# Kernel optimization log

Measured on AMD Instinct MI355X. Metric: run time of the kernel, lower is better.

## Reference

```python
import jax, jax.numpy as jnp
import numpy as np

V, H, T, B, S = 100000, 256, 11, 32, 512
START, STOP = 9, 10
NEG = -1000.0


def _lstm_dir(x, wih, whh, b, reverse):
    """One direction of one LSTM layer. x: [B,S,in] -> [B,S,H]. Gate order i,f,g,o (PyTorch)."""
    Bx = x.shape[0]
    Hh = whh.shape[1]
    xs = (jnp.einsum('bsi,gi->bsg', x, wih) + b).transpose(1, 0, 2)  # [S,B,4H]

    def step(carry, xt):
        h, c = carry
        g = xt + h @ whh.T
        i, f, gg, o = jnp.split(g, 4, axis=-1)
        c = jax.nn.sigmoid(f) * c + jax.nn.sigmoid(i) * jnp.tanh(gg)
        h = jax.nn.sigmoid(o) * jnp.tanh(c)
        return (h, c), h

    init = (jnp.zeros((Bx, Hh), x.dtype), jnp.zeros((Bx, Hh), x.dtype))
    _, hs = jax.lax.scan(step, init, xs, reverse=reverse)
    return hs.transpose(1, 0, 2)


def _viterbi(feats, trans):
    """Max-plus Viterbi decode. feats: [B,S,T]. trans[next,prev]."""
    Bx, Sx, Tx = feats.shape
    init = jnp.full((Bx, Tx), NEG, feats.dtype).at[:, START].set(0.0)

    def fwd_step(fv, feat_t):
        scores = fv[:, None, :] + trans[None, :, :]      # [B,next,prev]
        bp = jnp.argmax(scores, axis=2)                  # [B,T]
        fv = jnp.max(scores, axis=2) + feat_t
        return fv, bp

    fv, bptrs = jax.lax.scan(fwd_step, init, feats.transpose(1, 0, 2))  # bptrs [S,B,T]
    terminal = fv + trans[STOP][None, :]
    score = jnp.max(terminal, axis=1)
    last = jnp.argmax(terminal, axis=1)

    def back_step(tag, bp):
        prev = jnp.take_along_axis(bp, tag[:, None], axis=1)[:, 0]
        return prev, tag

    _, path = jax.lax.scan(back_step, last, bptrs, reverse=True)  # [S,B], path[t]=tag_t
    return score, path.T  # [B], [B,S]


def setup_inputs() -> dict:
    key = jax.random.key(0)
    ks = jax.random.split(key, 20)

    def n(k, shape, s=0.1):
        return jax.random.normal(k, shape, jnp.float32) * s

    inp = {}
    inp['x'] = jax.random.randint(ks[0], (B, S), 0, V, dtype=jnp.int32)
    inp['batch_seq_len'] = jnp.full((B,), S, jnp.int32)
    inp['emb'] = n(ks[1], (V, H), 1.0)
    # layer 0 (input H), layer 1 (input 2H); f/b directions; bias = b_ih + b_hh fused
    inp['wih0f'] = n(ks[2], (4 * H, H)); inp['whh0f'] = n(ks[3], (4 * H, H)); inp['b0f'] = n(ks[4], (4 * H,))
    inp['wih0b'] = n(ks[5], (4 * H, H)); inp['whh0b'] = n(ks[6], (4 * H, H)); inp['b0b'] = n(ks[7], (4 * H,))
    inp['wih1f'] = n(ks[8], (4 * H, 2 * H)); inp['whh1f'] = n(ks[9], (4 * H, H)); inp['b1f'] = n(ks[10], (4 * H,))
    inp['wih1b'] = n(ks[11], (4 * H, 2 * H)); inp['whh1b'] = n(ks[12], (4 * H, H)); inp['b1b'] = n(ks[13], (4 * H,))
    inp['w_out'] = n(ks[14], (T, 2 * H)); inp['b_out'] = n(ks[15], (T,))
    trans = jax.random.normal(ks[16], (T, T), jnp.float32)
    trans = trans.at[START, :].set(NEG).at[:, STOP].set(NEG)
    inp['trans'] = trans
    return inp


def reference(x, batch_seq_len, emb, wih0f, whh0f, b0f, wih0b, whh0b, b0b,
              wih1f, whh1f, b1f, wih1b, whh1b, b1b, w_out, b_out, trans):
    # batch_seq_len: all sequences full length -> pack/pad is a no-op
    xe = emb[x]                                            # [B,S,H]
    h = jnp.concatenate([_lstm_dir(xe, wih0f, whh0f, b0f, False),
                         _lstm_dir(xe, wih0b, whh0b, b0b, True)], axis=-1)
    h = jnp.concatenate([_lstm_dir(h, wih1f, whh1f, b1f, False),
                         _lstm_dir(h, wih1b, whh1b, b1b, True)], axis=-1)
    feats = jnp.einsum('bsh,th->bst', h, w_out) + b_out    # [B,S,T]
    score, tag_seq = _viterbi(feats, trans)
    return score, tag_seq
```

## Files before the change

### kernel.cpp

```cpp
#include <hip/hip_runtime.h>
#include <math.h>

#define SS 512
#define BB 32
#define HH 256
#define G4 1024
#define TT 11
#define NEGV (-1000.0f)

static const size_t OFF_XE    = 0;
static const size_t OFF_XS    = 16777216ull;
static const size_t OFF_H0    = OFF_XS + 134217728ull;
static const size_t OFF_H1    = OFF_H0 + 33554432ull;
static const size_t OFF_FEATS = OFF_H1 + 33554432ull;
static const size_t OFF_HGRP  = OFF_FEATS + 720896ull;

__device__ __forceinline__ float fsig(float x) {
  return __builtin_amdgcn_rcpf(1.f + __expf(-x));
}
__device__ __forceinline__ float ftanh(float x) {
  return 1.f - 2.f * __builtin_amdgcn_rcpf(__expf(2.f * x) + 1.f);
}

__device__ __forceinline__ void block_sync_lds() {
  asm volatile("s_waitcnt lgkmcnt(0)\n\ts_barrier" ::: "memory");
}

__global__ void emb_kernel(const int* __restrict__ x, const float4* __restrict__ emb,
                           float4* __restrict__ xe) {
  int idx = blockIdx.x * 256 + threadIdx.x;
  int bs  = idx >> 6;
  int kq  = idx & 63;
  int row = x[bs];
  xe[idx] = emb[(size_t)row * 64 + kq];
}

template<int K>
__global__ __launch_bounds__(256, 2)
void proj_kernel(const float* __restrict__ A,
                 const float* __restrict__ Wf, const float* __restrict__ Wb,
                 const float* __restrict__ bf, const float* __restrict__ bb,
                 float* __restrict__ xs) {
  __shared__ float As[8][132];
  __shared__ float Bs[8][132];
  int tid = threadIdx.x;
  int dir = blockIdx.z;
  const float* W    = dir ? Wb : Wf;
  const float* bias = dir ? bb : bf;
  float* out = xs + (size_t)dir * (SS * BB * G4);
  int bm = blockIdx.x * 128;
  int bn = blockIdx.y * 128;
  int ty = tid >> 4;
  int tx = tid & 15;
  int lr = tid >> 1;
  int lk = (tid & 1) * 4;
  const float* Ap = A + (size_t)(bm + lr) * K + lk;
  const float* Wp = W + (size_t)(bn + lr) * K + lk;
  float acc[8][8];
  #pragma unroll
  for (int i = 0; i < 8; i++)
    #pragma unroll
    for (int j = 0; j < 8; j++) acc[i][j] = 0.f;

  for (int kt = 0; kt < K; kt += 8) {
    float4 av = *(const float4*)(Ap + kt);
    float4 bv = *(const float4*)(Wp + kt);
    __syncthreads();
    As[lk + 0][lr] = av.x; As[lk + 1][lr] = av.y; As[lk + 2][lr] = av.z; As[lk + 3][lr] = av.w;
    Bs[lk + 0][lr] = bv.x; Bs[lk + 1][lr] = bv.y; Bs[lk + 2][lr] = bv.z; Bs[lk + 3][lr] = bv.w;
    __syncthreads();
    #pragma unroll
    for (int k = 0; k < 8; k++) {
      float4 a0 = *(const float4*)&As[k][ty * 8];
      float4 a1 = *(const float4*)&As[k][ty * 8 + 4];
      float4 b0 = *(const float4*)&Bs[k][tx * 8];
      float4 b1 = *(const float4*)&Bs[k][tx * 8 + 4];
      float a[8] = {a0.x, a0.y, a0.z, a0.w, a1.x, a1.y, a1.z, a1.w};
      float b[8] = {b0.x, b0.y, b0.z, b0.w, b1.x, b1.y, b1.z, b1.w};
      #pragma unroll
      for (int i = 0; i < 8; i++)
        #pragma unroll
        for (int j = 0; j < 8; j++)
          acc[i][j] += a[i] * b[j];
    }
  }
  int nb = bn + tx * 8;
  float4 bias0 = *(const float4*)(bias + nb);
  float4 bias1 = *(const float4*)(bias + nb + 4);
  #pragma unroll
  for (int i = 0; i < 8; i++) {
    int gm = bm + ty * 8 + i;
    int b_ = gm >> 9;
    int s_ = gm & 511;
    float* op = out + (size_t)(s_ * BB + b_) * G4 + nb;
    float4 v0, v1;
    v0.x = acc[i][0] + bias0.x; v0.y = acc[i][1] + bias0.y;
    v0.z = acc[i][2] + bias0.z; v0.w = acc[i][3] + bias0.w;
    v1.x = acc[i][4] + bias1.x; v1.y = acc[i][5] + bias1.y;
    v1.z = acc[i][6] + bias1.z; v1.w = acc[i][7] + bias1.w;
    *(float4*)op = v0;
    *(float4*)(op + 4) = v1;
  }
}

__global__ __launch_bounds__(320, 2)
void scan_kernel(const float* __restrict__ xs,
                 const float* __restrict__ whhf, const float* __restrict__ whhb,
                 unsigned long long* __restrict__ hgrp,
                 float* __restrict__ hout)
{
  int tid  = threadIdx.x;
  int w    = tid >> 6;
  int lane = tid & 63;
  int cg   = blockIdx.x;
  int g    = blockIdx.y;
  int dir  = blockIdx.z;
  const float* xsd = xs + (size_t)dir * (SS * BB * G4);
  unsigned long long* hg = hgrp + (size_t)(dir * 8 + g) * (2 * 4 * 256);

  __shared__ float h_sh[4][256];
  __shared__ float part[2][4][4][4][32];

  int c  = lane & 31;
  int bp = lane >> 5;

  if (w < 4) {
    const float* whh = dir ? whhb : whhf;
    int i0 = bp * 2;
    float4 wreg[2][16];
    #pragma unroll
    for (int i = 0; i < 2; i++) {
      int grow = (i0 + i) * 256 + cg * 32 + c;
      const float* wp = whh + (size_t)grow * 256 + w * 64;
      #pragma unroll
      for (int j = 0; j < 16; j++) wreg[i][j] = *(const float4*)(wp + j * 4);
    }
    int col = w * 64 + lane;

    for (int s = 0; s < SS; ++s) {
      const unsigned long long* src = hg + (size_t)(s & 1) * 1024 + col;
      unsigned long long rv0, rv1, rv2, rv3;
      for (;;) {
        rv0 = __hip_atomic_load(src,       __ATOMIC_RELAXED, __HIP_MEMORY_SCOPE_AGENT);
        rv1 = __hip_atomic_load(src + 256, __ATOMIC_RELAXED, __HIP_MEMORY_SCOPE_AGENT);
        rv2 = __hip_atomic_load(src + 512, __ATOMIC_RELAXED, __HIP_MEMORY_SCOPE_AGENT);
        rv3 = __hip_atomic_load(src + 768, __ATOMIC_RELAXED, __HIP_MEMORY_SCOPE_AGENT);
        unsigned t = ((unsigned)(rv0 >> 32) ^ (unsigned)s) |
                     ((unsigned)(rv1 >> 32) ^ (unsigned)s) |
                     ((unsigned)(rv2 >> 32) ^ (unsigned)s) |
                     ((unsigned)(rv3 >> 32) ^ (unsigned)s);
        if (__all(t == 0u)) break;
      }
      {
        unsigned l0 = (unsigned)rv0, l1 = (unsigned)rv1,
                 l2 = (unsigned)rv2, l3 = (unsigned)rv3;
        float f0, f1, f2, f3;
        __builtin_memcpy(&f0, &l0, 4); __builtin_memcpy(&f1, &l1, 4);
        __builtin_memcpy(&f2, &l2, 4); __builtin_memcpy(&f3, &l3, 4);
        h_sh[0][col] = f0; h_sh[1][col] = f1;
        h_sh[2][col] = f2; h_sh[3][col] = f3;
      }

      float acc[2][4] = {{0.f,0.f,0.f,0.f},{0.f,0.f,0.f,0.f}};
      #pragma unroll
      for (int j = 0; j < 16; j++) {
        int k4 = w * 64 + j * 4;
        float4 hb0 = *(const float4*)&h_sh[0][k4];
        float4 hb1 = *(const float4*)&h_sh[1][k4];
        float4 hb2 = *(const float4*)&h_sh[2][k4];
        float4 hb3 = *(const float4*)&h_sh[3][k4];
        #pragma unroll
        for (int i = 0; i < 2; i++) {
          float4 wv = wreg[i][j];
          acc[i][0] += wv.x * hb0.x + wv.y * hb0.y + wv.z * hb0.z + wv.w * hb0.w;
          acc[i][1] += wv.x * hb1.x + wv.y * hb1.y + wv.z * hb1.z + wv.w * hb1.w;
          acc[i][2] += wv.x * hb2.x + wv.y * hb2.y + wv.z * hb2.z + wv.w * hb2.w;
          acc[i][3] += wv.x * hb3.x + wv.y * hb3.y + wv.z * hb3.z + wv.w * hb3.w;
        }
      }
      #pragma unroll
      for (int i = 0; i < 2; i++)
        #pragma unroll
        for (int b = 0; b < 4; b++)
          part[s & 1][w][b][i0 + i][c] = acc[i][b];

      block_sync_lds();
    }
  } else {
    int b0l = bp * 2;
    int gb0 = g * 4 + b0l, gb1 = gb0 + 1;
    int colp = cg * 32 + c;
    float c0 = 0.f, c1 = 0.f;
    float xg0[4], xg1[4];
    {
      int tpos = dir ? (SS - 1) : 0;
      const float* xp0 = xsd + (size_t)(tpos * BB + gb0) * G4 + colp;
      const float* xp1 = xsd + (size_t)(tpos * BB + gb1) * G4 + colp;
      #pragma unroll
      for (int i = 0; i < 4; i++) { xg0[i] = xp0[i * 256]; xg1[i] = xp1[i * 256]; }
    }

    for (int s = 0; s < SS; ++s) {
      block_sync_lds();

      float gv0[4], gv1[4];
      #pragma unroll
      for (int i = 0; i < 4; i++) {
        float s0 = xg0[i], s1 = xg1[i];
        #pragma unroll
        for (int ww = 0; ww < 4; ww++) {
          s0 += part[s & 1][ww][b0l][i][c];
          s1 += part[s & 1][ww][b0l + 1][i][c];
        }
        gv0[i] = s0; gv1[i] = s1;
      }
      float hv0, hv1;
      { float ig = fsig(gv0[0]), fg = fsig(gv0[1]);
        float gg = ftanh(gv0[2]), og = fsig(gv0[3]);
        c0 = fg * c0 + ig * gg; hv0 = og * ftanh(c0); }
      { float ig = fsig(gv1[0]), fg = fsig(gv1[1]);
        float gg = ftanh(gv1[2]), og = fsig(gv1[3]);
        c1 = fg * c1 + ig * gg; hv1 = og * ftanh(c1); }

      unsigned hb0, hb1;
      __builtin_memcpy(&hb0, &hv0, 4); __builtin_memcpy(&hb1, &hv1, 4);
      unsigned long long tagw = (unsigned long long)(unsigned)(s + 1) << 32;
      unsigned long long* dst = hg + (size_t)((s + 1) & 1) * 1024 + colp;
      __hip_atomic_store(dst + (size_t)b0l * 256,      tagw | hb0,
                         __ATOMIC_RELAXED, __HIP_MEMORY_SCOPE_AGENT);
      __hip_atomic_store(dst + (size_t)(b0l + 1) * 256, tagw | hb1,
                         __ATOMIC_RELAXED, __HIP_MEMORY_SCOPE_AGENT);

      int tpos = dir ? (SS - 1 - s) : s;
      hout[((size_t)(gb0 * SS + tpos)) * 512 + dir * 256 + colp] = hv0;
      hout[((size_t)(gb1 * SS + tpos)) * 512 + dir * 256 + colp] = hv1;

      if (s + 1 < SS) {
        int tpn = dir ? (SS - 2 - s) : (s + 1);
        const float* xp0 = xsd + (size_t)(tpn * BB + gb0) * G4 + colp;
        const float* xp1 = xsd + (size_t)(tpn * BB + gb1) * G4 + colp;
        #pragma unroll
        for (int i = 0; i < 4; i++) { xg0[i] = xp0[i * 256]; xg1[i] = xp1[i * 256]; }
      }
    }
  }
}

__global__ void feats_kernel(const float* __restrict__ h1, const float* __restrict__ wout,
                             const float* __restrict__ bout, float* __restrict__ feats) {
  int bs = blockIdx.x;
  int lane = threadIdx.x;
  const float* hp = h1 + (size_t)bs * 512;
  float hv[8];
  #pragma unroll
  for (int i = 0; i < 8; i++) hv[i] = hp[lane + i * 64];
  #pragma unroll
  for (int t = 0; t < TT; t++) {
    const float* wp = wout + t * 512;
    float p = 0.f;
    #pragma unroll
    for (int i = 0; i < 8; i++) p += hv[i] * wp[lane + i * 64];
    #pragma unroll
    for (int off = 32; off >= 1; off >>= 1) p += __shfl_down(p, off, 64);
    if (lane == 0) feats[(size_t)bs * TT + t] = p + bout[t];
  }
}

__global__ void viterbi_kernel(const float* __restrict__ feats, const float* __restrict__ trans,
                               float* __restrict__ out) {
  int b = blockIdx.x;
  int lane = threadIdx.x;
  __shared__ float tr[121];
  __shared__ float fch[32 * TT];
  __shared__ unsigned char bp[SS][12];
  __shared__ unsigned char path[SS];
  for (int i = lane; i < 121; i += 64) tr[i] = trans[i];
  __syncthreads();
  int ln = lane < TT ? lane : (TT - 1);
  float trr[TT];
  #pragma unroll
  for (int p = 0; p < TT; p++) trr[p] = tr[ln * TT + p];
  float fv = (lane == 9) ? 0.f : NEGV;
  const float* fb = feats + (size_t)b * SS * TT;

  for (int s = 0; s < SS; s++) {
    if ((s & 31) == 0) {
      __syncthreads();
      for (int i = lane; i < 32 * TT; i += 64) fch[i] = fb[s * TT + i];
      __syncthreads();
    }
    float best = -3.0e38f; int arg = 0;
    #pragma unroll
    for (int p = 0; p < TT; p++) {
      float v = __shfl(fv, p, 64) + trr[p];
      if (v > best) { best = v; arg = p; }
    }
    if (lane < TT) bp[s][lane] = (unsigned char)arg;
    fv = best + fch[(s & 31) * TT + ln];
  }
  float term = fv + tr[10 * TT + ln];
  float best = -3.0e38f; int arg = 0;
  #pragma unroll
  for (int p = 0; p < TT; p++) {
    float v = __shfl(term, p, 64);
    if (v > best) { best = v; arg = p; }
  }
  __syncthreads();
  if (lane == 0) {
    out[b] = best;
    int tg = arg;
    path[SS - 1] = (unsigned char)tg;
    for (int s = SS - 1; s >= 1; s--) {
      tg = bp[s][tg];
      path[s - 1] = (unsigned char)tg;
    }
  }
  __syncthreads();
  for (int i = lane; i < SS; i += 64) out[32 + b * SS + i] = (float)path[i];
}

extern "C" void kernel_launch(void* const* d_in, const int* in_sizes, int n_in,
                              void* d_out, int out_size, void* d_ws, size_t ws_size,
                              hipStream_t stream) {
  const int*   x     = (const int*)d_in[0];
  const float* emb   = (const float*)d_in[2];
  const float* wih0f = (const float*)d_in[3];
  const float* whh0f = (const float*)d_in[4];
  const float* b0f   = (const float*)d_in[5];
  const float* wih0b = (const float*)d_in[6];
  const float* whh0b = (const float*)d_in[7];
  const float* b0b   = (const float*)d_in[8];
  const float* wih1f = (const float*)d_in[9];
  const float* whh1f = (const float*)d_in[10];
  const float* b1f   = (const float*)d_in[11];
  const float* wih1b = (const float*)d_in[12];
  const float* whh1b = (const float*)d_in[13];
  const float* b1b   = (const float*)d_in[14];
  const float* wout  = (const float*)d_in[15];
  const float* bout  = (const float*)d_in[16];
  const float* trans = (const float*)d_in[17];

  char* ws = (char*)d_ws;
  float* xe    = (float*)(ws + OFF_XE);
  float* xs    = (float*)(ws + OFF_XS);
  float* h0    = (float*)(ws + OFF_H0);
  float* h1    = (float*)(ws + OFF_H1);
  float* feats = (float*)(ws + OFF_FEATS);
  unsigned long long* hgrp = (unsigned long long*)(ws + OFF_HGRP);
  float* outp  = (float*)d_out;

  emb_kernel<<<4096, 256, 0, stream>>>(x, (const float4*)emb, (float4*)xe);
  proj_kernel<256><<<dim3(128, 8, 2), 256, 0, stream>>>(xe, wih0f, wih0b, b0f, b0b, xs);
  hipMemsetAsync(hgrp, 0, 1048576, stream);
  scan_kernel<<<dim3(8, 8, 2), 320, 0, stream>>>(xs, whh0f, whh0b, hgrp, h0);
  proj_kernel<512><<<dim3(128, 8, 2), 256, 0, stream>>>(h0, wih1f, wih1b, b1f, b1b, xs);
  hipMemsetAsync(hgrp, 0, 1048576, stream);
  scan_kernel<<<dim3(8, 8, 2), 320, 0, stream>>>(xs, whh1f, whh1b, hgrp, h1);
  feats_kernel<<<BB * SS, 64, 0, stream>>>(h1, wout, bout, feats);
  viterbi_kernel<<<BB, 64, 0, stream>>>(feats, trans, outp);
}
```

Before: 3.848 ms.

## Run input projections on bf16 MFMA with hi/lo split for fp32 accuracy

Replaces the fp32 FMA tiled GEMM for both layers' input projections with an MFMA 16x16x32 bf16 kernel. Each operand is split into high and low bf16 parts and four MFMAs are accumulated, which approximates fp32 precision. New split kernels convert the weights, the embeddings and the layer-0 output into bf16 pairs. This adds conversion passes, extra memory traffic and 4x MFMA work, in exchange for offloading the projection GEMMs from the vector ALUs to the matrix units. The dominant recurrent scan is left untouched.

```diff
diff --git a/kernel.cpp b/kernel.cpp
--- a/kernel.cpp
+++ b/kernel.cpp
@@ -8,12 +8,20 @@
 #define TT 11
 #define NEGV (-1000.0f)
 
-static const size_t OFF_XE    = 0;
+static const size_t OFF_XEH   = 0;
+static const size_t OFF_XEL   = 8388608ull;
 static const size_t OFF_XS    = 16777216ull;
 static const size_t OFF_H0    = OFF_XS + 134217728ull;
 static const size_t OFF_H1    = OFF_H0 + 33554432ull;
 static const size_t OFF_FEATS = OFF_H1 + 33554432ull;
 static const size_t OFF_HGRP  = OFF_FEATS + 720896ull;
+static const size_t OFF_W0H   = OFF_HGRP + 1048576ull;
+static const size_t OFF_W0L   = OFF_W0H + 1048576ull;
+static const size_t OFF_W1H   = OFF_W0L + 1048576ull;
+static const size_t OFF_W1L   = OFF_W1H + 2097152ull;
+
+typedef __attribute__((ext_vector_type(8))) short short8;
+typedef __attribute__((ext_vector_type(4))) float f32x4;
 
 __device__ __forceinline__ float fsig(float x) {
   return __builtin_amdgcn_rcpf(1.f + __expf(-x));
@@ -26,81 +34,118 @@
   asm volatile("s_waitcnt lgkmcnt(0)\n\ts_barrier" ::: "memory");
 }
 
+__device__ __forceinline__ unsigned short bfh(float x) {
+  unsigned u = __float_as_uint(x);
+  unsigned r = u + 0x7fffu + ((u >> 16) & 1u);
+  return (unsigned short)(r >> 16);
+}
+__device__ __forceinline__ void split1(float x, unsigned short& h, unsigned short& l) {
+  h = bfh(x);
+  float hf = __uint_as_float(((unsigned)h) << 16);
+  l = bfh(x - hf);
+}
+
 __global__ void emb_kernel(const int* __restrict__ x, const float4* __restrict__ emb,
-                           float4* __restrict__ xe) {
+                           ushort4* __restrict__ xeh, ushort4* __restrict__ xel) {
   int idx = blockIdx.x * 256 + threadIdx.x;
   int bs  = idx >> 6;
   int kq  = idx & 63;
-  int row = x[bs];
-  xe[idx] = emb[(size_t)row * 64 + kq];
+  float4 v = emb[(size_t)x[bs] * 64 + kq];
+  ushort4 h, l;
+  split1(v.x, h.x, l.x); split1(v.y, h.y, l.y);
+  split1(v.z, h.z, l.z); split1(v.w, h.w, l.w);
+  xeh[idx] = h; xel[idx] = l;
+}
+
+__global__ void split_kernel(const float4* __restrict__ in, ushort4* __restrict__ oh,
+                             ushort4* __restrict__ ol, int n4) {
+  int i = blockIdx.x * 256 + threadIdx.x;
+  if (i < n4) {
+    float4 v = in[i];
+    ushort4 h, l;
+    split1(v.x, h.x, l.x); split1(v.y, h.y, l.y);
+    split1(v.z, h.z, l.z); split1(v.w, h.w, l.w);
+    oh[i] = h; ol[i] = l;
+  }
 }
 
 template<int K>
 __global__ __launch_bounds__(256, 2)
-void proj_kernel(const float* __restrict__ A,
-                 const float* __restrict__ Wf, const float* __restrict__ Wb,
-                 const float* __restrict__ bf, const float* __restrict__ bb,
-                 float* __restrict__ xs) {
-  __shared__ float As[8][132];
-  __shared__ float Bs[8][132];
+void proj_mfma(const unsigned short* __restrict__ Ah_g, const unsigned short* __restrict__ Al_g,
+               const unsigned short* __restrict__ Wh_g, const unsigned short* __restrict__ Wl_g,
+               const float* __restrict__ bf, const float* __restrict__ bb,
+               float* __restrict__ xs) {
   int tid = threadIdx.x;
+  int bm  = blockIdx.x * 64;
+  int bn  = blockIdx.y * 128;
   int dir = blockIdx.z;
-  const float* W    = dir ? Wb : Wf;
+  const unsigned short* Wh = Wh_g + (size_t)dir * 1024 * K;
+  const unsigned short* Wl = Wl_g + (size_t)dir * 1024 * K;
   const float* bias = dir ? bb : bf;
   float* out = xs + (size_t)dir * (SS * BB * G4);
-  int bm = blockIdx.x * 128;
-  int bn = blockIdx.y * 128;
-  int ty = tid >> 4;
-  int tx = tid & 15;
-  int lr = tid >> 1;
-  int lk = (tid & 1) * 4;
-  const float* Ap = A + (size_t)(bm + lr) * K + lk;
-  const float* Wp = W + (size_t)(bn + lr) * K + lk;
-  float acc[8][8];
-  #pragma unroll
-  for (int i = 0; i < 8; i++)
-    #pragma unroll
-    for (int j = 0; j < 8; j++) acc[i][j] = 0.f;
-
-  for (int kt = 0; kt < K; kt += 8) {
-    float4 av = *(const float4*)(Ap + kt);
-    float4 bv = *(const float4*)(Wp + kt);
+
+  __shared__ unsigned short AhS[64][40], AlS[64][40];
+  __shared__ unsigned short BhS[128][40], BlS[128][40];
+
+  int w = tid >> 6, lane = tid & 63;
+  int wm = w >> 1, wn = w & 1;
+  int fr = lane & 15, q8 = (lane >> 4) * 8;
+  int ra = tid >> 2;
+  int ck = (tid & 3) * 8;
+
+  f32x4 acc[2][4];
+  #pragma unroll
+  for (int mt = 0; mt < 2; mt++)
+    #pragma unroll
+    for (int nt = 0; nt < 4; nt++) acc[mt][nt] = 0;
+
+  for (int k0 = 0; k0 < K; k0 += 32) {
     __syncthreads();
-    As[lk + 0][lr] = av.x; As[lk + 1][lr] = av.y; As[lk + 2][lr] = av.z; As[lk + 3][lr] = av.w;
-    Bs[lk + 0][lr] = bv.x; Bs[lk + 1][lr] = bv.y; Bs[lk + 2][lr] = bv.z; Bs[lk + 3][lr] = bv.w;
+    *(uint4*)&AhS[ra][ck] = *(const uint4*)(Ah_g + (size_t)(bm + ra) * K + k0 + ck);
+    *(uint4*)&AlS[ra][ck] = *(const uint4*)(Al_g + (size_t)(bm + ra) * K + k0 + ck);
+    *(uint4*)&BhS[ra][ck]      = *(const uint4*)(Wh + (size_t)(bn + ra) * K + k0 + ck);
+    *(uint4*)&BhS[ra + 64][ck] = *(const uint4*)(Wh + (size_t)(bn + ra + 64) * K + k0 + ck);
+    *(uint4*)&BlS[ra][ck]      = *(const uint4*)(Wl + (size_t)(bn + ra) * K + k0 + ck);
+    *(uint4*)&BlS[ra + 64][ck] = *(const uint4*)(Wl + (size_t)(bn + ra + 64) * K + k0 + ck);
     __syncthreads();
-    #pragma unroll
-    for (int k = 0; k < 8; k++) {
-      float4 a0 = *(const float4*)&As[k][ty * 8];
-      float4 a1 = *(const float4*)&As[k][ty * 8 + 4];
-      float4 b0 = *(const float4*)&Bs[k][tx * 8];
-      float4 b1 = *(const float4*)&Bs[k][tx * 8 + 4];
-      float a[8] = {a0.x, a0.y, a0.z, a0.w, a1.x, a1.y, a1.z, a1.w};
-      float b[8] = {b0.x, b0.y, b0.z, b0.w, b1.x, b1.y, b1.z, b1.w};
-      #pragma unroll
-      for (int i = 0; i < 8; i++)
-        #pragma unroll
-        for (int j = 0; j < 8; j++)
-          acc[i][j] += a[i] * b[j];
-    }
-  }
-  int nb = bn + tx * 8;
-  float4 bias0 = *(const float4*)(bias + nb);
-  float4 bias1 = *(const float4*)(bias + nb + 4);
-  #pragma unroll
-  for (int i = 0; i < 8; i++) {
-    int gm = bm + ty * 8 + i;
-    int b_ = gm >> 9;
-    int s_ = gm & 511;
-    float* op = out + (size_t)(s_ * BB + b_) * G4 + nb;
-    float4 v0, v1;
-    v0.x = acc[i][0] + bias0.x; v0.y = acc[i][1] + bias0.y;
-    v0.z = acc[i][2] + bias0.z; v0.w = acc[i][3] + bias0.w;
-    v1.x = acc[i][4] + bias1.x; v1.y = acc[i][5] + bias1.y;
-    v1.z = acc[i][6] + bias1.z; v1.w = acc[i][7] + bias1.w;
-    *(float4*)op = v0;
-    *(float4*)(op + 4) = v1;
-  }
+
+    short8 ah[2], al[2], bh[4], bl[4];
+    #pragma unroll
+    for (int mt = 0; mt < 2; mt++) {
+      ah[mt] = *(const short8*)&AhS[wm * 32 + mt * 16 + fr][q8];
+      al[mt] = *(const short8*)&AlS[wm * 32 + mt * 16 + fr][q8];
+    }
+    #pragma unroll
+    for (int nt = 0; nt < 4; nt++) {
+      bh[nt] = *(const short8*)&BhS[wn * 64 + nt * 16 + fr][q8];
+      bl[nt] = *(const short8*)&BlS[wn * 64 + nt * 16 + fr][q8];
+    }
+    #pragma unroll
+    for (int mt = 0; mt < 2; mt++)
+      #pragma unroll
+      for (int nt = 0; nt < 4; nt++) {
+        acc[mt][nt] = __builtin_amdgcn_mfma_f32_16x16x32_bf16(ah[mt], bh[nt], acc[mt][nt], 0, 0, 0);
+        acc[mt][nt] = __builtin_amdgcn_mfma_f32_16x16x32_bf16(ah[mt], bl[nt], acc[mt][nt], 0, 0, 0);
+        acc[mt][nt] = __builtin_amdgcn_mfma_f32_16x16x32_bf16(al[mt], bh[nt], acc[mt][nt], 0, 0, 0);
+        acc[mt][nt] = __builtin_amdgcn_mfma_f32_16x16x32_bf16(al[mt], bl[nt], acc[mt][nt], 0, 0, 0);
+      }
+  }
+
+  #pragma unroll
+  for (int mt = 0; mt < 2; mt++)
+    #pragma unroll
+    for (int nt = 0; nt < 4; nt++) {
+      int n  = bn + wn * 64 + nt * 16 + fr;
+      float bv = bias[n];
+      int mbase = bm + wm * 32 + mt * 16 + (lane >> 4) * 4;
+      #pragma unroll
+      for (int r = 0; r < 4; r++) {
+        int mm = mbase + r;
+        int b_ = mm >> 9;
+        int s_ = mm & 511;
+        out[(size_t)(s_ * BB + b_) * G4 + n] = acc[mt][nt][r] + bv;
+      }
+    }
 }
 
 __global__ __launch_bounds__(320, 2)
@@ -341,21 +386,38 @@
   const float* trans = (const float*)d_in[17];
 
   char* ws = (char*)d_ws;
-  float* xe    = (float*)(ws + OFF_XE);
+  unsigned short* xeh = (unsigned short*)(ws + OFF_XEH);
+  unsigned short* xel = (unsigned short*)(ws + OFF_XEL);
   float* xs    = (float*)(ws + OFF_XS);
   float* h0    = (float*)(ws + OFF_H0);
   float* h1    = (float*)(ws + OFF_H1);
+  unsigned short* h0h = (unsigned short*)(ws + OFF_H1);
+  unsigned short* h0l = (unsigned short*)(ws + OFF_H1 + 16777216ull);
   float* feats = (float*)(ws + OFF_FEATS);
   unsigned long long* hgrp = (unsigned long long*)(ws + OFF_HGRP);
+  unsigned short* w0h = (unsigned short*)(ws + OFF_W0H);
+  unsigned short* w0l = (unsigned short*)(ws + OFF_W0L);
+  unsigned short* w1h = (unsigned short*)(ws + OFF_W1H);
+  unsigned short* w1l = (unsigned short*)(ws + OFF_W1L);
   float* outp  = (float*)d_out;
 
-  emb_kernel<<<4096, 256, 0, stream>>>(x, (const float4*)emb, (float4*)xe);
-  proj_kernel<256><<<dim3(128, 8, 2), 256, 0, stream>>>(xe, wih0f, wih0b, b0f, b0b, xs);
+  emb_kernel<<<4096, 256, 0, stream>>>(x, (const float4*)emb, (ushort4*)xeh, (ushort4*)xel);
+  split_kernel<<<256, 256, 0, stream>>>((const float4*)wih0f, (ushort4*)w0h, (ushort4*)w0l, 65536);
+  split_kernel<<<256, 256, 0, stream>>>((const float4*)wih0b, (ushort4*)(w0h + 262144),
+                                        (ushort4*)(w0l + 262144), 65536);
+  split_kernel<<<512, 256, 0, stream>>>((const float4*)wih1f, (ushort4*)w1h, (ushort4*)w1l, 131072);
+  split_kernel<<<512, 256, 0, stream>>>((const float4*)wih1b, (ushort4*)(w1h + 524288),
+                                        (ushort4*)(w1l + 524288), 131072);
+
+  proj_mfma<256><<<dim3(256, 8, 2), 256, 0, stream>>>(xeh, xel, w0h, w0l, b0f, b0b, xs);
   hipMemsetAsync(hgrp, 0, 1048576, stream);
   scan_kernel<<<dim3(8, 8, 2), 320, 0, stream>>>(xs, whh0f, whh0b, hgrp, h0);
-  proj_kernel<512><<<dim3(128, 8, 2), 256, 0, stream>>>(h0, wih1f, wih1b, b1f, b1b, xs);
+
+  split_kernel<<<8192, 256, 0, stream>>>((const float4*)h0, (ushort4*)h0h, (ushort4*)h0l, 2097152);
+  proj_mfma<512><<<dim3(256, 8, 2), 256, 0, stream>>>(h0h, h0l, w1h, w1l, b1f, b1b, xs);
   hipMemsetAsync(hgrp, 0, 1048576, stream);
   scan_kernel<<<dim3(8, 8, 2), 320, 0, stream>>>(xs, whh1f, whh1b, hgrp, h1);
+
   feats_kernel<<<BB * SS, 64, 0, stream>>>(h1, wout, bout, feats);
   viterbi_kernel<<<BB, 64, 0, stream>>>(feats, trans, outp);
 }
```

Measured after the change: 3.489 ms. 1.1x faster.
